# Kernel optimization log

Hardware: AMD Instinct MI355X
Metric: run time of the kernel (lower is better)

Reference implementation:

```python
import jax, jax.numpy as jnp
import numpy as np


def _segment_sparsemax(x, batch, B):
    """Per-group sparsemax over a flat ragged tensor.

    x: [N] float values; batch: [N] sorted int group ids in [0, B).
    Groups are contiguous, so an in-group descending sort is a stable
    lexsort on (batch, -x); per-group cumsum is a global cumsum minus the
    cumsum value just before each group's start offset.
    """
    N = x.shape[0]
    num_nodes = jax.ops.segment_sum(jnp.ones(N, jnp.int32), batch, num_segments=B)  # [B]
    start = jnp.concatenate([jnp.zeros(1, jnp.int32), jnp.cumsum(num_nodes)[:-1]])  # [B]

    # shift by per-group max for numerical stability (as in torch forward)
    gmax = jax.ops.segment_max(x, batch, num_segments=B)
    xs = x - gmax[batch]

    # descending sort within each contiguous group
    order = jnp.lexsort((-xs, batch))
    sx = xs[order]  # [N], group-wise descending; group layout unchanged

    # per-group cumulative sum via global cumsum + start offsets
    cs = jnp.cumsum(sx)
    off = jnp.where(start > 0, cs[jnp.maximum(start - 1, 0)], jnp.zeros((), sx.dtype))  # [B]
    seg_cs = cs - off[batch] - 1.0  # input_cumsum - 1.0

    # rho = 1..n_g within each group
    rho = (jnp.arange(N, dtype=jnp.int32) - start[batch] + 1).astype(xs.dtype)

    support = rho * sx > seg_cs  # [N] bool
    supp_size = jax.ops.segment_sum(support.astype(jnp.int32), batch, num_segments=B)  # [B]

    idx = jnp.maximum(supp_size + start - 1, 0)  # [B]
    tau = seg_cs[idx] / supp_size.astype(xs.dtype)  # [B]

    return jnp.maximum(xs - tau[batch], 0.0)


def setup_inputs() -> dict:
    key = jax.random.key(0)
    k1, k2 = jax.random.split(key)
    N = 8_388_608
    B = 4096
    x = jax.random.normal(k1, (N,), dtype=jnp.float32)
    batch = jnp.sort(jax.random.randint(k2, (N,), 0, B)).astype(jnp.int64)
    return {"x": x, "batch": batch, "num_groups": B}


def reference(x, batch, num_groups):
    batch = batch.astype(jnp.int32)
    return _segment_sparsemax(x, batch, int(num_groups))
```

## Files before the change

kernel.cpp:

```cpp
#include <hip/hip_runtime.h>

#define BLK 256
#define WPT 10
#define WCAP (WPT * 64 * 4)
#define CCAP 320


__device__ __forceinline__ float wave_max(float v) {
#pragma unroll
  for (int o = 32; o; o >>= 1) v = fmaxf(v, __shfl_xor(v, o));
  return v;
}
__device__ __forceinline__ float wave_sum(float v) {
#pragma unroll
  for (int o = 32; o; o >>= 1) v += __shfl_xor(v, o);
  return v;
}
__device__ __forceinline__ int wave_sum_i(int v) {
#pragma unroll
  for (int o = 32; o; o >>= 1) v += __shfl_xor(v, o);
  return v;
}


extern "C" __global__ void __launch_bounds__(256)
build_starts(const int* __restrict__ batch, int* __restrict__ starts,
             const int* __restrict__ pB, int N) {
  const int B = *pB;
  const long long tid = (long long)blockIdx.x * 256 + threadIdx.x;
  const long long i0 = tid * 8;
  if (i0 >= N) return;
  int v[8];
  if (i0 + 8 <= N) {
    const int4 a = *(const int4*)(batch + i0);
    const int4 b = *(const int4*)(batch + i0 + 4);
    v[0] = a.x; v[1] = a.y; v[2] = a.z; v[3] = a.w;
    v[4] = b.x; v[5] = b.y; v[6] = b.z; v[7] = b.w;
  } else {
#pragma unroll
    for (int t = 0; t < 8; ++t) v[t] = (i0 + t < N) ? batch[i0 + t] : 0;
  }
  int prev = (i0 == 0) ? -1 : batch[i0 - 1];
#pragma unroll
  for (int t = 0; t < 8; ++t) {
    if (i0 + t >= N) break;
    const int cur = v[t];
    for (int g = prev + 1; g <= cur; ++g) starts[g] = (int)(i0 + t);
    prev = cur;
  }
  if (i0 + 8 >= N) {
    for (int g = prev + 1; g <= B; ++g) starts[g] = N;
  }
}


extern "C" __global__ void __launch_bounds__(BLK)
sparsemax_groups(const float* __restrict__ x, const int* __restrict__ starts,
                 const int* __restrict__ pB, float* __restrict__ out, int N) {
  __shared__ float cand[4][CCAP];
  __shared__ float sorted_[4][64];
  const int tid  = threadIdx.x;
  const int lane = tid & 63;
  const int w    = tid >> 6;
  const int B = *pB;

  for (int g = blockIdx.x * 4 + w; g < B; g += gridDim.x * 4) {
    const int s = starts[g];
    const int e = starts[g + 1];
    const int n = e - s;
    if (n <= 0) continue;
    const int a0 = s & ~3;

    if (e - a0 <= WCAP) {
      float4 r[WPT];
      float lmax = -INFINITY;
#pragma unroll
      for (int j = 0; j < WPT; ++j) {
        const int idx = a0 + (j * 64 + lane) * 4;
        float4 v = make_float4(-INFINITY, -INFINITY, -INFINITY, -INFINITY);
        if (idx < e) {
          if (idx + 4 <= N) {
            v = *(const float4*)(x + idx);
          } else {
            if (idx + 0 < N) v.x = x[idx + 0];
            if (idx + 1 < N) v.y = x[idx + 1];
            if (idx + 2 < N) v.z = x[idx + 2];
            if (idx + 3 < N) v.w = x[idx + 3];
          }
          if (idx + 0 < s || idx + 0 >= e) v.x = -INFINITY;
          if (idx + 1 < s || idx + 1 >= e) v.y = -INFINITY;
          if (idx + 2 < s || idx + 2 >= e) v.z = -INFINITY;
          if (idx + 3 < s || idx + 3 >= e) v.w = -INFINITY;
        }
        r[j] = v;
        lmax = fmaxf(lmax, fmaxf(fmaxf(v.x, v.y), fmaxf(v.z, v.w)));
      }
      const float gmax = wave_max(lmax);
      const float thr = gmax - 1.0f;

      int cnt = 0;
      float wsum = 0.0f;
#pragma unroll
      for (int j = 0; j < WPT; ++j) {
        const float vv[4] = {r[j].x, r[j].y, r[j].z, r[j].w};
#pragma unroll
        for (int t = 0; t < 4; ++t) {
          const bool p = vv[t] > thr;
          const unsigned long long bal = __ballot(p);
          if (bal) {
            if (p) {
              const int off = cnt + __popcll(bal & ((1ull << lane) - 1ull));
              if (off < CCAP) cand[w][off] = vv[t];
              wsum += vv[t] - gmax;
            }
            cnt += __popcll(bal);
          }
        }
      }
      wsum = wave_sum(wsum);
      const int c = cnt;

      float tau;
      if (c <= 64) {
        const float v = (lane < c) ? cand[w][lane] - gmax : 0.0f;
        int rank = 0;
        for (int q = 0; q < c; ++q) {
          const float t = cand[w][q] - gmax;
          rank += (t > v) || (t == v && q < lane);
        }
        if (lane < c) sorted_[w][rank] = v;
        const float sv = (lane < c) ? sorted_[w][lane] : 0.0f;
        float cs = sv;
#pragma unroll
        for (int o = 1; o < 64; o <<= 1) {
          const float t2 = __shfl_up(cs, o);
          if (lane >= o) cs += t2;
        }
        const int flag = (lane < c) && (sv * (float)(lane + 1) > cs - 1.0f);
        const unsigned long long bal2 = __ballot(flag);
        const int k = 63 - __clzll(bal2);
        const float csk = __shfl(cs, k);
        tau = (csk - 1.0f) / (float)(k + 1);
      } else if (c <= CCAP) {
        tau = (wsum - 1.0f) / (float)c;
        int cnt2 = c;
        for (int it = 0; it < 64; ++it) {
          float s2 = 0.0f; int c2 = 0;
          for (int q = lane; q < c; q += 64) {
            const float vs = cand[w][q] - gmax;
            if (vs > tau) { s2 += vs; c2++; }
          }
          s2 = wave_sum(s2); c2 = wave_sum_i(c2);
          if (c2 == cnt2 || c2 == 0) break;
          tau = (s2 - 1.0f) / (float)c2; cnt2 = c2;
        }
      } else {
        tau = (wsum - 1.0f) / (float)c;
        int cnt2 = c;
        for (int it = 0; it < 64; ++it) {
          float s2 = 0.0f; int c2 = 0;
#pragma unroll
          for (int j = 0; j < WPT; ++j) {
            const float vv[4] = {r[j].x, r[j].y, r[j].z, r[j].w};
#pragma unroll
            for (int t = 0; t < 4; ++t) {
              const float vs = vv[t] - gmax;
              if (vs > tau) { s2 += vs; c2++; }
            }
          }
          s2 = wave_sum(s2); c2 = wave_sum_i(c2);
          if (c2 == cnt2 || c2 == 0) break;
          tau = (s2 - 1.0f) / (float)c2; cnt2 = c2;
        }
      }

      const float sub = tau + gmax;

#pragma unroll
      for (int j = 0; j < WPT; ++j) {
        const int idx = a0 + (j * 64 + lane) * 4;
        if (idx >= e) continue;
        if (idx >= s && idx + 4 <= e) {
          float4 o4;
          o4.x = fmaxf(r[j].x - sub, 0.0f);
          o4.y = fmaxf(r[j].y - sub, 0.0f);
          o4.z = fmaxf(r[j].z - sub, 0.0f);
          o4.w = fmaxf(r[j].w - sub, 0.0f);
          *(float4*)(out + idx) = o4;
        } else {
          const float vv[4] = {r[j].x, r[j].y, r[j].z, r[j].w};
#pragma unroll
          for (int t = 0; t < 4; ++t) {
            const int p2 = idx + t;
            if (p2 >= s && p2 < e) out[p2] = fmaxf(vv[t] - sub, 0.0f);
          }
        }
      }
    } else {
      float gmax = -INFINITY;
      for (int i = s + lane; i < e; i += 64) gmax = fmaxf(gmax, x[i]);
      gmax = wave_max(gmax);
      float bs = 0.0f; int bc = 0;
      for (int i = s + lane; i < e; i += 64) {
        const float vs = x[i] - gmax;
        if (vs > -1.0f) { bs += vs; bc++; }
      }
      bs = wave_sum(bs); bc = wave_sum_i(bc);
      float tau = (bs - 1.0f) / (float)bc;
      int cntS = bc;
      for (int it = 0; it < 64; ++it) {
        float s2 = 0.0f; int c2 = 0;
        for (int i = s + lane; i < e; i += 64) {
          const float vs = x[i] - gmax;
          if (vs > tau) { s2 += vs; c2++; }
        }
        s2 = wave_sum(s2); c2 = wave_sum_i(c2);
        if (c2 == cntS || c2 == 0) break;
        tau = (s2 - 1.0f) / (float)c2; cntS = c2;
      }
      const float sub = tau + gmax;
      for (int i = s + lane; i < e; i += 64) out[i] = fmaxf(x[i] - sub, 0.0f);
    }
  }
}

extern "C" void kernel_launch(void* const* d_in, const int* in_sizes, int n_in,
                              void* d_out, int out_size, void* d_ws, size_t ws_size,
                              hipStream_t stream) {
  const float* x     = (const float*)d_in[0];
  const int*   batch = (const int*)d_in[1];
  const int*   pB    = (const int*)d_in[2];
  float*       out   = (float*)d_out;
  const int N = in_sizes[0];

  int* starts = (int*)d_ws;

  const int g1 = (N + 2047) / 2048;
  build_starts<<<dim3(g1), dim3(256), 0, stream>>>(batch, starts, pB, N);
  sparsemax_groups<<<dim3(1024), dim3(BLK), 0, stream>>>(x, starts, pB, out, N);
}
```

Before: 113.4 us.

## Fuse group-boundary search into sparsemax kernel via windowed binary search

Removes the separate pass that scanned the whole batch array to build group start offsets. Each wave now finds its group's start and end with a binary search over the sorted batch array, using half-waves for the two bounds. The search is first restricted to a window around the uniform estimate. This avoids a full read of the batch array and one kernel launch, in exchange for a few dependent latency-bound loads per group.

```diff
diff --git a/kernel.cpp b/kernel.cpp
--- a/kernel.cpp
+++ b/kernel.cpp
@@ -4,6 +4,7 @@
 #define WPT 10
 #define WCAP (WPT * 64 * 4)
 #define CCAP 320
+#define SWIN 8192
 
 
 __device__ __forceinline__ float wave_max(float v) {
@@ -23,40 +24,23 @@
 }
 
 
-extern "C" __global__ void __launch_bounds__(256)
-build_starts(const int* __restrict__ batch, int* __restrict__ starts,
-             const int* __restrict__ pB, int N) {
-  const int B = *pB;
-  const long long tid = (long long)blockIdx.x * 256 + threadIdx.x;
-  const long long i0 = tid * 8;
-  if (i0 >= N) return;
-  int v[8];
-  if (i0 + 8 <= N) {
-    const int4 a = *(const int4*)(batch + i0);
-    const int4 b = *(const int4*)(batch + i0 + 4);
-    v[0] = a.x; v[1] = a.y; v[2] = a.z; v[3] = a.w;
-    v[4] = b.x; v[5] = b.y; v[6] = b.z; v[7] = b.w;
-  } else {
-#pragma unroll
-    for (int t = 0; t < 8; ++t) v[t] = (i0 + t < N) ? batch[i0 + t] : 0;
+__device__ __forceinline__ int lower_bound_win(const int* __restrict__ batch,
+                                               int N, int b, int est) {
+  int lo = est - SWIN; if (lo < 0) lo = 0;
+  int hi = est + SWIN; if (hi > N) hi = N;
+  if (lo > 0 && batch[lo - 1] >= b) lo = 0;
+  if (hi < N && batch[hi] < b) hi = N;
+  while (lo < hi) {
+    const int mid = (lo + hi) >> 1;
+    if (batch[mid] < b) lo = mid + 1; else hi = mid;
   }
-  int prev = (i0 == 0) ? -1 : batch[i0 - 1];
-#pragma unroll
-  for (int t = 0; t < 8; ++t) {
-    if (i0 + t >= N) break;
-    const int cur = v[t];
-    for (int g = prev + 1; g <= cur; ++g) starts[g] = (int)(i0 + t);
-    prev = cur;
-  }
-  if (i0 + 8 >= N) {
-    for (int g = prev + 1; g <= B; ++g) starts[g] = N;
-  }
+  return lo;
 }
 
 
 extern "C" __global__ void __launch_bounds__(BLK)
-sparsemax_groups(const float* __restrict__ x, const int* __restrict__ starts,
-                 const int* __restrict__ pB, float* __restrict__ out, int N) {
+sparsemax_fused(const float* __restrict__ x, const int* __restrict__ batch,
+                const int* __restrict__ pB, float* __restrict__ out, int N) {
   __shared__ float cand[4][CCAP];
   __shared__ float sorted_[4][64];
   const int tid  = threadIdx.x;
@@ -65,8 +49,11 @@
   const int B = *pB;
 
   for (int g = blockIdx.x * 4 + w; g < B; g += gridDim.x * 4) {
-    const int s = starts[g];
-    const int e = starts[g + 1];
+    const int b   = g + (lane >= 32 ? 1 : 0);
+    const int est = (int)(((long long)b * N) / B);
+    const int sb  = lower_bound_win(batch, N, b, est);
+    const int s   = __shfl(sb, 0);
+    const int e   = __shfl(sb, 32);
     const int n = e - s;
     if (n <= 0) continue;
     const int a0 = s & ~3;
@@ -233,9 +220,6 @@
   float*       out   = (float*)d_out;
   const int N = in_sizes[0];
 
-  int* starts = (int*)d_ws;
-
-  const int g1 = (N + 2047) / 2048;
-  build_starts<<<dim3(g1), dim3(256), 0, stream>>>(batch, starts, pB, N);
-  sparsemax_groups<<<dim3(1024), dim3(BLK), 0, stream>>>(x, starts, pB, out, N);
-}
+  (void)d_ws; (void)ws_size;
+  sparsemax_fused<<<dim3(1024), dim3(BLK), 0, stream>>>(x, batch, pB, out, N);
+}
```

New measurement: 125.2 us. 10.5% more time.

## Build group starts by sampling batch ids every 64 elements

Applied to the files above, without the earlier changes.

Replaces the full scan of the batch array with a sampled scan: one wave lane reads every 64th batch id, and only intervals whose endpoints differ are rescanned in full by a wave to find the exact boundaries. With about 4096 groups over 8M elements, most intervals hold no boundary, so far less of the 32 MB index array needs to be read. It depends on the batch array being sorted and adds serial per-interval loops inside each wave.

```diff
diff --git a/kernel.cpp b/kernel.cpp
--- a/kernel.cpp
+++ b/kernel.cpp
@@ -4,6 +4,7 @@
 #define WPT 10
 #define WCAP (WPT * 64 * 4)
 #define CCAP 320
+#define SSTR 64
 
 
 __device__ __forceinline__ float wave_max(float v) {
@@ -24,32 +25,49 @@
 
 
 extern "C" __global__ void __launch_bounds__(256)
-build_starts(const int* __restrict__ batch, int* __restrict__ starts,
-             const int* __restrict__ pB, int N) {
+build_starts_sampled(const int* __restrict__ batch, int* __restrict__ starts,
+                     const int* __restrict__ pB, int N) {
   const int B = *pB;
-  const long long tid = (long long)blockIdx.x * 256 + threadIdx.x;
-  const long long i0 = tid * 8;
-  if (i0 >= N) return;
-  int v[8];
-  if (i0 + 8 <= N) {
-    const int4 a = *(const int4*)(batch + i0);
-    const int4 b = *(const int4*)(batch + i0 + 4);
-    v[0] = a.x; v[1] = a.y; v[2] = a.z; v[3] = a.w;
-    v[4] = b.x; v[5] = b.y; v[6] = b.z; v[7] = b.w;
-  } else {
-#pragma unroll
-    for (int t = 0; t < 8; ++t) v[t] = (i0 + t < N) ? batch[i0 + t] : 0;
-  }
-  int prev = (i0 == 0) ? -1 : batch[i0 - 1];
-#pragma unroll
-  for (int t = 0; t < 8; ++t) {
-    if (i0 + t >= N) break;
-    const int cur = v[t];
-    for (int g = prev + 1; g <= cur; ++g) starts[g] = (int)(i0 + t);
-    prev = cur;
-  }
-  if (i0 + 8 >= N) {
-    for (int g = prev + 1; g <= B; ++g) starts[g] = N;
+  const int lane = threadIdx.x & 63;
+  const int w    = threadIdx.x >> 6;
+  const int wgid = blockIdx.x * 4 + w;
+  const int K = (N + SSTR - 1) / SSTR;
+
+  if (wgid == 0 && lane == 0) {
+    const int b0 = batch[0];
+    for (int g = 0; g <= b0; ++g) starts[g] = 0;
+    const int bl = batch[N - 1];
+    for (int g = bl + 1; g <= B; ++g) starts[g] = N;
+  }
+
+  const int kbase = wgid * 64;
+  if (kbase >= K) return;
+  const int k = kbase + lane;
+
+  const long long p0 = (long long)k * SSTR;
+  const int v0 = batch[(p0 < N) ? p0 : (N - 1)];
+  int v1 = __shfl(v0, lane + 1);
+  if (lane == 63) {
+    const long long p1 = (long long)(k + 1) * SSTR;
+    v1 = batch[(p1 < N) ? p1 : (N - 1)];
+  }
+  const bool changed = (k < K) && (v0 != v1);
+  unsigned long long m = __ballot(changed);
+
+  while (m) {
+    const int i = __ffsll((long long)m) - 1;
+    m &= m - 1;
+    const int vA = __shfl(v0, i);
+    const long long A = (long long)(kbase + i) * SSTR;
+    const long long idx = A + 1 + lane;
+    const bool act = idx < N;
+    int c = vA;
+    if (act) c = batch[idx];
+    int pv = __shfl_up(c, 1);
+    if (lane == 0) pv = vA;
+    if (act && pv != c) {
+      for (int g = pv + 1; g <= c; ++g) starts[g] = (int)idx;
+    }
   }
 }
 
@@ -235,7 +253,8 @@
 
   int* starts = (int*)d_ws;
 
-  const int g1 = (N + 2047) / 2048;
-  build_starts<<<dim3(g1), dim3(256), 0, stream>>>(batch, starts, pB, N);
+  const int K  = (N + SSTR - 1) / SSTR;
+  const int g1 = (K + 255) / 256;
+  build_starts_sampled<<<dim3(g1), dim3(256), 0, stream>>>(batch, starts, pB, N);
   sparsemax_groups<<<dim3(1024), dim3(BLK), 0, stream>>>(x, starts, pB, out, N);
 }
```

Result: slower. 118.9 us (+4.9%).
